# Performance work log

Hardware: AMD Instinct MI355X
Metric: run time of the kernel (lower is better)

Reference implementation:

```python
import jax, jax.numpy as jnp
import numpy as np
from math import sqrt

B, S, D = 4, 2048, 1024


def setup_inputs() -> dict:
    key = jax.random.key(0)
    k1, k2, k3, k4 = jax.random.split(key, 4)
    scale = 1.0 / sqrt(D)  # roughly nn.Linear init magnitude
    x = jax.random.normal(k1, (B, S, D), dtype=jnp.float32)
    Wq = jax.random.normal(k2, (D, D), dtype=jnp.float32) * scale
    Wk = jax.random.normal(k3, (D, D), dtype=jnp.float32) * scale
    Wv = jax.random.normal(k4, (D, D), dtype=jnp.float32) * scale
    attn_mask = jnp.ones((B, S), dtype=jnp.int32)  # 1 = attend, 0 = pad
    return {"x": x, "attn_mask": attn_mask, "Wq": Wq, "Wk": Wk, "Wv": Wv}


def reference(x, attn_mask, Wq, Wk, Wv):
    # torch nn.Linear: y = x @ W.T (no bias)
    q = jnp.einsum("bsd,ed->bse", x, Wq)
    k = jnp.einsum("bsd,ed->bse", x, Wk)
    v = jnp.einsum("bsd,ed->bse", x, Wv)

    scores = jnp.einsum("bqd,bkd->bqk", q, k)  # [B, S, S]

    # causal mask (upper triangle above diagonal masked out)
    causal_mask = jnp.triu(jnp.ones((S, S), dtype=bool), k=1)  # [S, S]
    scores = jnp.where(causal_mask[None, :, :], -jnp.inf, scores)

    # padding mask: attn_mask [B, S] broadcast over query dim
    pad = (attn_mask == 0)[:, None, :]  # [B, 1, S]
    scores = jnp.where(pad, -jnp.inf, scores)

    attn_weights = jax.nn.softmax(scores / sqrt(D), axis=-1)
    return jnp.einsum("bqk,bkd->bqd", attn_weights, v)
```

## Files before the change

### kernel.cpp

```cpp
#include <hip/hip_runtime.h>
#include <stdint.h>
#include <math.h>

#define BATCH 4
#define SEQ   2048
#define DIM   1024

#define BK 32
#define LSTR 32

typedef __attribute__((ext_vector_type(8))) short short8;
typedef __attribute__((ext_vector_type(4))) float floatx4;

typedef __attribute__((address_space(3))) unsigned int lds_u32;
typedef const __attribute__((address_space(1))) unsigned int glb_u32;

__device__ __forceinline__ unsigned short f2bf(float f) {
    union { float f; unsigned u; } x; x.f = f;
    unsigned r = x.u + 0x7fffu + ((x.u >> 16) & 1u);
    return (unsigned short)(r >> 16);
}

__global__ void cvt_kernel(const float* __restrict__ x,
                           const float* __restrict__ wq,
                           const float* __restrict__ wk,
                           const float* __restrict__ wv,
                           unsigned short* __restrict__ xb,
                           unsigned short* __restrict__ wb) {
    int i4 = (blockIdx.x * 256 + threadIdx.x) * 4;
    const float* src; unsigned short* dst; int off;
    if (i4 < 8388608)       { src = x;  dst = xb;            off = i4; }
    else if (i4 < 9437184)  { src = wq; dst = wb;            off = i4 - 8388608; }
    else if (i4 < 10485760) { src = wk; dst = wb + 1048576;  off = i4 - 9437184; }
    else                    { src = wv; dst = wb + 2097152;  off = i4 - 10485760; }
    float4 v = *(const float4*)(src + off);
    ushort4 o;
    o.x = f2bf(v.x); o.y = f2bf(v.y); o.z = f2bf(v.z); o.w = f2bf(v.w);
    *(ushort4*)(dst + off) = o;
}

__device__ __forceinline__ void stage_async(unsigned short* sh, const unsigned short* g,
                                            int ld, int tid) {
#pragma unroll
    for (int it = 0; it < 2; ++it) {
        int c = it * 256 + tid;
        int row = c >> 2, cc = c & 3;
        __builtin_amdgcn_global_load_lds(
            (glb_u32*)(g + (size_t)row * ld + cc * 8),
            (lds_u32*)(sh + c * 8), 16, 0, 0);
    }
}

__device__ __forceinline__ void mfma_step(const unsigned short* Ash, const unsigned short* Bsh,
                                          int lane, int wr, int wc, floatx4 acc[4][4]) {
    int lrow = lane & 15, lq = lane >> 4;
    short8 af[4], bf[4];
#pragma unroll
    for (int i = 0; i < 4; ++i) {
        af[i] = *(const short8*)(Ash + (wr * 64 + i * 16 + lrow) * LSTR + lq * 8);
        bf[i] = *(const short8*)(Bsh + (wc * 64 + i * 16 + lrow) * LSTR + lq * 8);
    }
#pragma unroll
    for (int i = 0; i < 4; ++i)
#pragma unroll
        for (int j = 0; j < 4; ++j)
            acc[i][j] = __builtin_amdgcn_mfma_f32_16x16x32_bf16(af[i], bf[j], acc[i][j], 0, 0, 0);
}

__global__ __launch_bounds__(256) void qkv_gemm(const unsigned short* __restrict__ Xb,
                                                const unsigned short* __restrict__ Wb,
                                                unsigned short* __restrict__ Qb,
                                                unsigned short* __restrict__ Kb,
                                                unsigned short* __restrict__ Vt) {
    __shared__ unsigned short Ash[128 * LSTR];
    __shared__ unsigned short Bsh[128 * LSTR];
    int tid = threadIdx.x;
    int bm = blockIdx.x, bn = blockIdx.y;
    int lane = tid & 63, w = tid >> 6, wr = w >> 1, wc = w & 1;
    floatx4 acc[4][4];
#pragma unroll
    for (int i = 0; i < 4; ++i)
#pragma unroll
        for (int j = 0; j < 4; ++j) acc[i][j] = (floatx4){0.f, 0.f, 0.f, 0.f};

    const unsigned short* Ag = Xb + (size_t)bm * 128 * 1024;
    const unsigned short* Bg = Wb + (size_t)bn * 128 * 1024;
    for (int k0 = 0; k0 < 1024; k0 += BK) {
        __syncthreads();
        stage_async(Ash, Ag + k0, 1024, tid);
        stage_async(Bsh, Bg + k0, 1024, tid);
        __syncthreads();
        mfma_step(Ash, Bsh, lane, wr, wc, acc);
    }

    int lrow = lane & 15, lq = lane >> 4;
#pragma unroll
    for (int i = 0; i < 4; ++i) {
        int mbase = bm * 128 + wr * 64 + i * 16 + lq * 4;
#pragma unroll
        for (int j = 0; j < 4; ++j) {
            int n = bn * 128 + wc * 64 + j * 16 + lrow;
            int which = n >> 10, nn = n & 1023;
            if (which == 0) {
#pragma unroll
                for (int r = 0; r < 4; ++r)
                    Qb[(size_t)(mbase + r) * 1024 + nn] = f2bf(acc[i][j][r]);
            } else if (which == 1) {
#pragma unroll
                for (int r = 0; r < 4; ++r)
                    Kb[(size_t)(mbase + r) * 1024 + nn] = f2bf(acc[i][j][r]);
            } else {
                int b = mbase >> 11, s = mbase & 2047;
                ushort4 o;
                o.x = f2bf(acc[i][j][0]); o.y = f2bf(acc[i][j][1]);
                o.z = f2bf(acc[i][j][2]); o.w = f2bf(acc[i][j][3]);
                *(ushort4*)(Vt + ((size_t)b * 1024 + nn) * 2048 + s) = o;
            }
        }
    }
}

__global__ __launch_bounds__(256) void scores_gemm(const unsigned short* __restrict__ Qb,
                                                   const unsigned short* __restrict__ Kb,
                                                   const int* __restrict__ mask,
                                                   float* __restrict__ Sf) {
    int u = blockIdx.x, b = blockIdx.y;
    int ti = (int)((sqrtf(8.0f * (float)u + 1.0f) - 1.0f) * 0.5f);
    while ((ti + 1) * (ti + 2) / 2 <= u) ti++;
    while (ti * (ti + 1) / 2 > u) ti--;
    int tj = u - ti * (ti + 1) / 2;

    __shared__ unsigned short Ash[128 * LSTR];
    __shared__ unsigned short Bsh[128 * LSTR];
    int tid = threadIdx.x;
    int lane = tid & 63, w = tid >> 6, wr = w >> 1, wc = w & 1;
    floatx4 acc[4][4];
#pragma unroll
    for (int i = 0; i < 4; ++i)
#pragma unroll
        for (int j = 0; j < 4; ++j) acc[i][j] = (floatx4){0.f, 0.f, 0.f, 0.f};

    const unsigned short* Ag = Qb + ((size_t)b * 2048 + ti * 128) * 1024;
    const unsigned short* Bg = Kb + ((size_t)b * 2048 + tj * 128) * 1024;
    for (int k0 = 0; k0 < 1024; k0 += BK) {
        __syncthreads();
        stage_async(Ash, Ag + k0, 1024, tid);
        stage_async(Bsh, Bg + k0, 1024, tid);
        __syncthreads();
        mfma_step(Ash, Bsh, lane, wr, wc, acc);
    }

    float* Srow = Sf + (size_t)b * 2048 * 2048;
    int lrow = lane & 15, lq = lane >> 4;
#pragma unroll
    for (int i = 0; i < 4; ++i) {
        int qrow = ti * 128 + wr * 64 + i * 16 + lq * 4;
#pragma unroll
        for (int j = 0; j < 4; ++j) {
            int n = tj * 128 + wc * 64 + j * 16 + lrow;
            int mk = mask[b * 2048 + n];
#pragma unroll
            for (int r = 0; r < 4; ++r) {
                int q = qrow + r;
                float v = acc[i][j][r] * 0.03125f;
                if (n > q || mk == 0) v = -INFINITY;
                Srow[(size_t)q * 2048 + n] = v;
            }
        }
    }
}

__global__ __launch_bounds__(256) void softmax_k(float* __restrict__ Sf) {
    int bid = blockIdx.x;
    int q = bid & 2047;
    int t = threadIdx.x;
    float* row = Sf + (size_t)bid * 2048;
    unsigned short* prow = (unsigned short*)row;
    int Lw = ((q >> 7) + 1) << 7;
    int base = t * 8;
    bool act = base < Lw;
    float v[8];
    if (act) {
        float4 a = *(const float4*)(row + base);
        float4 c = *(const float4*)(row + base + 4);
        v[0] = a.x; v[1] = a.y; v[2] = a.z; v[3] = a.w;
        v[4] = c.x; v[5] = c.y; v[6] = c.z; v[7] = c.w;
    } else {
#pragma unroll
        for (int r = 0; r < 8; ++r) v[r] = -INFINITY;
    }
    float m = -INFINITY;
#pragma unroll
    for (int r = 0; r < 8; ++r) m = fmaxf(m, v[r]);
#pragma unroll
    for (int o = 32; o >= 1; o >>= 1) m = fmaxf(m, __shfl_xor(m, o));
    __shared__ float red[4];
    if ((t & 63) == 0) red[t >> 6] = m;
    __syncthreads();
    m = fmaxf(fmaxf(red[0], red[1]), fmaxf(red[2], red[3]));

    float s = 0.f;
    if (act) {
#pragma unroll
        for (int r = 0; r < 8; ++r) { v[r] = __expf(v[r] - m); s += v[r]; }
    }
#pragma unroll
    for (int o = 32; o >= 1; o >>= 1) s += __shfl_xor(s, o);
    __syncthreads();
    if ((t & 63) == 0) red[t >> 6] = s;
    __syncthreads();
    s = red[0] + red[1] + red[2] + red[3];
    float inv = 1.f / s;
    if (act) {
        union { ushort4 u4[2]; unsigned short u[8]; } o;
#pragma unroll
        for (int r = 0; r < 8; ++r) o.u[r] = f2bf(v[r] * inv);
        *(ushort4*)(prow + base) = o.u4[0];
        *(ushort4*)(prow + base + 4) = o.u4[1];
    }
}

__global__ __launch_bounds__(256) void pv_gemm(const unsigned short* __restrict__ Pb,
                                               const unsigned short* __restrict__ Vt,
                                               float* __restrict__ out) {
    int bid = blockIdx.x;
    int ti = 15 - (bid >> 5);
    int dj = (bid >> 2) & 7;
    int b  = bid & 3;
    __shared__ unsigned short Ash[128 * LSTR];
    __shared__ unsigned short Bsh[128 * LSTR];
    int tid = threadIdx.x;
    int lane = tid & 63, w = tid >> 6, wr = w >> 1, wc = w & 1;
    floatx4 acc[4][4];
#pragma unroll
    for (int i = 0; i < 4; ++i)
#pragma unroll
        for (int j = 0; j < 4; ++j) acc[i][j] = (floatx4){0.f, 0.f, 0.f, 0.f};

    const unsigned short* Ag = Pb + ((size_t)b * 2048 + ti * 128) * 4096;
    const unsigned short* Bg = Vt + ((size_t)b * 1024 + dj * 128) * 2048;
    int kend = (ti + 1) * 128;
    for (int k0 = 0; k0 < kend; k0 += BK) {
        __syncthreads();
        stage_async(Ash, Ag + k0, 4096, tid);
        stage_async(Bsh, Bg + k0, 2048, tid);
        __syncthreads();
        mfma_step(Ash, Bsh, lane, wr, wc, acc);
    }

    int lrow = lane & 15, lq = lane >> 4;
#pragma unroll
    for (int i = 0; i < 4; ++i) {
        int qrow = ti * 128 + wr * 64 + i * 16 + lq * 4;
#pragma unroll
        for (int j = 0; j < 4; ++j) {
            int d = dj * 128 + wc * 64 + j * 16 + lrow;
#pragma unroll
            for (int r = 0; r < 4; ++r)
                out[((size_t)b * 2048 + qrow + r) * 1024 + d] = acc[i][j][r];
        }
    }
}

extern "C" void kernel_launch(void* const* d_in, const int* in_sizes, int n_in,
                              void* d_out, int out_size, void* d_ws, size_t ws_size,
                              hipStream_t stream) {
    const float* x    = (const float*)d_in[0];
    const int*   mask = (const int*)d_in[1];
    const float* wq   = (const float*)d_in[2];
    const float* wk   = (const float*)d_in[3];
    const float* wv   = (const float*)d_in[4];
    float* out = (float*)d_out;
    char* ws = (char*)d_ws;

    unsigned short* Xb = (unsigned short*)(ws + 0);
    unsigned short* Wb = (unsigned short*)(ws + 16777216);
    unsigned short* Qb = (unsigned short*)(ws + 23068672);
    unsigned short* Kb = (unsigned short*)(ws + 39845888);
    unsigned short* Vt = (unsigned short*)(ws + 56623104);
    float*          Sf = (float*)(ws + 73400320);
    (void)ws_size; (void)in_sizes; (void)n_in; (void)out_size;

    cvt_kernel<<<11264, 256, 0, stream>>>(x, wq, wk, wv, Xb, Wb);
    qkv_gemm<<<dim3(64, 24), 256, 0, stream>>>(Xb, Wb, Qb, Kb, Vt);
    scores_gemm<<<dim3(136, 4), 256, 0, stream>>>(Qb, Kb, mask, Sf);
    softmax_k<<<8192, 256, 0, stream>>>(Sf);
    pv_gemm<<<512, 256, 0, stream>>>((const unsigned short*)Sf, Vt, out);
}
```

Baseline: 251.1 us.

## Deepen K tile to 64 with XOR-swizzled LDS and LDS-staged coalesced QKV stores

Raises the K step of every GEMM from 32 to 64, which halves the number of barrier-separated stage/compute iterations. An XOR swizzle is applied to both the global-to-LDS async copy and the fragment reads to avoid LDS bank conflicts. The QKV epilogue now transposes tiles through a padded LDS buffer so Q, K and the transposed V are written with wide coalesced 16-byte stores instead of scattered 2-byte writes. The PV grid order is also remapped: the first half of the blocks run from the heaviest row tiles downward, the second half from the lightest upward. The cost is larger shared-memory tiles and an extra epilogue barrier.

```diff
diff --git a/kernel.cpp b/kernel.cpp
--- a/kernel.cpp
+++ b/kernel.cpp
@@ -2,12 +2,9 @@
 #include <stdint.h>
 #include <math.h>
 
-#define BATCH 4
-#define SEQ   2048
-#define DIM   1024
-
-#define BK 32
-#define LSTR 32
+#define BK 64
+#define LSTR 64
+#define ETS 132
 
 typedef __attribute__((ext_vector_type(8))) short short8;
 typedef __attribute__((ext_vector_type(4))) float floatx4;
@@ -42,11 +39,12 @@
 __device__ __forceinline__ void stage_async(unsigned short* sh, const unsigned short* g,
                                             int ld, int tid) {
 #pragma unroll
-    for (int it = 0; it < 2; ++it) {
+    for (int it = 0; it < 4; ++it) {
         int c = it * 256 + tid;
-        int row = c >> 2, cc = c & 3;
+        int row = c >> 3, cc = c & 7;
+        int gcc = cc ^ (row & 7);
         __builtin_amdgcn_global_load_lds(
-            (glb_u32*)(g + (size_t)row * ld + cc * 8),
+            (glb_u32*)(g + (size_t)row * ld + gcc * 8),
             (lds_u32*)(sh + c * 8), 16, 0, 0);
     }
 }
@@ -54,17 +52,22 @@
 __device__ __forceinline__ void mfma_step(const unsigned short* Ash, const unsigned short* Bsh,
                                           int lane, int wr, int wc, floatx4 acc[4][4]) {
     int lrow = lane & 15, lq = lane >> 4;
-    short8 af[4], bf[4];
-#pragma unroll
-    for (int i = 0; i < 4; ++i) {
-        af[i] = *(const short8*)(Ash + (wr * 64 + i * 16 + lrow) * LSTR + lq * 8);
-        bf[i] = *(const short8*)(Bsh + (wc * 64 + i * 16 + lrow) * LSTR + lq * 8);
-    }
-#pragma unroll
-    for (int i = 0; i < 4; ++i)
-#pragma unroll
-        for (int j = 0; j < 4; ++j)
-            acc[i][j] = __builtin_amdgcn_mfma_f32_16x16x32_bf16(af[i], bf[j], acc[i][j], 0, 0, 0);
+#pragma unroll
+    for (int h = 0; h < 2; ++h) {
+        short8 af[4], bf[4];
+#pragma unroll
+        for (int i = 0; i < 4; ++i) {
+            int ar = wr * 64 + i * 16 + lrow;
+            int br = wc * 64 + i * 16 + lrow;
+            af[i] = *(const short8*)(Ash + ar * LSTR + (((h << 2) | lq) ^ (ar & 7)) * 8);
+            bf[i] = *(const short8*)(Bsh + br * LSTR + (((h << 2) | lq) ^ (br & 7)) * 8);
+        }
+#pragma unroll
+        for (int i = 0; i < 4; ++i)
+#pragma unroll
+            for (int j = 0; j < 4; ++j)
+                acc[i][j] = __builtin_amdgcn_mfma_f32_16x16x32_bf16(af[i], bf[j], acc[i][j], 0, 0, 0);
+    }
 }
 
 __global__ __launch_bounds__(256) void qkv_gemm(const unsigned short* __restrict__ Xb,
@@ -72,8 +75,9 @@
                                                 unsigned short* __restrict__ Qb,
                                                 unsigned short* __restrict__ Kb,
                                                 unsigned short* __restrict__ Vt) {
-    __shared__ unsigned short Ash[128 * LSTR];
-    __shared__ unsigned short Bsh[128 * LSTR];
+    __shared__ unsigned short shbuf[128 * ETS];
+    unsigned short* Ash = shbuf;
+    unsigned short* Bsh = shbuf + 128 * LSTR;
     int tid = threadIdx.x;
     int bm = blockIdx.x, bn = blockIdx.y;
     int lane = tid & 63, w = tid >> 6, wr = w >> 1, wc = w & 1;
@@ -93,30 +97,43 @@
         mfma_step(Ash, Bsh, lane, wr, wc, acc);
     }
 
+    int which = bn >> 3;
+    int nnb = (bn & 7) * 128;
     int lrow = lane & 15, lq = lane >> 4;
-#pragma unroll
-    for (int i = 0; i < 4; ++i) {
-        int mbase = bm * 128 + wr * 64 + i * 16 + lq * 4;
-#pragma unroll
-        for (int j = 0; j < 4; ++j) {
-            int n = bn * 128 + wc * 64 + j * 16 + lrow;
-            int which = n >> 10, nn = n & 1023;
-            if (which == 0) {
+    __syncthreads();
+    if (which < 2) {
+#pragma unroll
+        for (int i = 0; i < 4; ++i)
+#pragma unroll
+            for (int j = 0; j < 4; ++j)
 #pragma unroll
                 for (int r = 0; r < 4; ++r)
-                    Qb[(size_t)(mbase + r) * 1024 + nn] = f2bf(acc[i][j][r]);
-            } else if (which == 1) {
-#pragma unroll
-                for (int r = 0; r < 4; ++r)
-                    Kb[(size_t)(mbase + r) * 1024 + nn] = f2bf(acc[i][j][r]);
-            } else {
-                int b = mbase >> 11, s = mbase & 2047;
+                    shbuf[(wr * 64 + i * 16 + lq * 4 + r) * ETS + wc * 64 + j * 16 + lrow] =
+                        f2bf(acc[i][j][r]);
+    } else {
+#pragma unroll
+        for (int i = 0; i < 4; ++i)
+#pragma unroll
+            for (int j = 0; j < 4; ++j) {
                 ushort4 o;
                 o.x = f2bf(acc[i][j][0]); o.y = f2bf(acc[i][j][1]);
                 o.z = f2bf(acc[i][j][2]); o.w = f2bf(acc[i][j][3]);
-                *(ushort4*)(Vt + ((size_t)b * 1024 + nn) * 2048 + s) = o;
+                *(ushort4*)(shbuf + (wc * 64 + j * 16 + lrow) * ETS + wr * 64 + i * 16 + lq * 4) = o;
             }
-        }
+    }
+    __syncthreads();
+
+    unsigned short* gbase; size_t gld;
+    if (which == 0)      { gbase = Qb + (size_t)(bm * 128) * 1024 + nnb; gld = 1024; }
+    else if (which == 1) { gbase = Kb + (size_t)(bm * 128) * 1024 + nnb; gld = 1024; }
+    else { gbase = Vt + ((size_t)(bm >> 4) * 1024 + nnb) * 2048 + (bm & 15) * 128; gld = 2048; }
+#pragma unroll
+    for (int it = 0; it < 4; ++it) {
+        int row = it * 32 + (tid >> 3), cc = tid & 7;
+        uint4 v0 = *(const uint4*)(shbuf + row * ETS + cc * 8);
+        uint4 v1 = *(const uint4*)(shbuf + row * ETS + 64 + cc * 8);
+        *(uint4*)(gbase + (size_t)row * gld + cc * 8) = v0;
+        *(uint4*)(gbase + (size_t)row * gld + 64 + cc * 8) = v1;
     }
 }
 
@@ -130,8 +147,9 @@
     while (ti * (ti + 1) / 2 > u) ti--;
     int tj = u - ti * (ti + 1) / 2;
 
-    __shared__ unsigned short Ash[128 * LSTR];
-    __shared__ unsigned short Bsh[128 * LSTR];
+    __shared__ unsigned short shbuf[2 * 128 * LSTR];
+    unsigned short* Ash = shbuf;
+    unsigned short* Bsh = shbuf + 128 * LSTR;
     int tid = threadIdx.x;
     int lane = tid & 63, w = tid >> 6, wr = w >> 1, wc = w & 1;
     floatx4 acc[4][4];
@@ -224,11 +242,14 @@
                                                const unsigned short* __restrict__ Vt,
                                                float* __restrict__ out) {
     int bid = blockIdx.x;
-    int ti = 15 - (bid >> 5);
-    int dj = (bid >> 2) & 7;
-    int b  = bid & 3;
-    __shared__ unsigned short Ash[128 * LSTR];
-    __shared__ unsigned short Bsh[128 * LSTR];
+    int half = bid >> 8, rr = bid & 255;
+    int tig = rr >> 5;
+    int ti = half ? tig : 15 - tig;
+    int dj = (rr >> 2) & 7;
+    int b  = rr & 3;
+    __shared__ unsigned short shbuf[2 * 128 * LSTR];
+    unsigned short* Ash = shbuf;
+    unsigned short* Bsh = shbuf + 128 * LSTR;
     int tid = threadIdx.x;
     int lane = tid & 63, w = tid >> 6, wr = w >> 1, wc = w & 1;
     floatx4 acc[4][4];
```

Result: no change. 252.9 us (+0.7%).
